# Kernel optimization log

Hardware: AMD Instinct MI355X
Metric: run time of the kernel (lower is better)

The kernel has to match this reference:

```python
import jax, jax.numpy as jnp
import numpy as np

B = 8
H_IN, W_IN = 448, 448
STRIDE = 32
NUM_CLASSES = 20
CONF_THRESH = 0.01
NMS_THRESH = 0.5
HS, WS = H_IN // STRIDE, W_IN // STRIDE  # 14, 14
N_CELLS = HS * WS  # 196
CHANNELS = [3, 64, 128, 256, 512, 512]
HEAD_OUT = 1 + NUM_CLASSES + 4  # 25


def _conv(x, w, stride):
    return jax.lax.conv_general_dilated(
        x, w, (stride, stride), 'SAME',
        dimension_numbers=('NCHW', 'OIHW', 'NCHW'))


def _create_grid():
    gy, gx = jnp.meshgrid(jnp.arange(HS), jnp.arange(WS), indexing='ij')
    return jnp.stack([gx, gy], -1).reshape(1, N_CELLS, 2).astype(jnp.float32)


def _iou_matrix(boxes):
    # boxes: [N,4] xyxy -> [N,N] pairwise IoU
    x1, y1, x2, y2 = boxes[:, 0], boxes[:, 1], boxes[:, 2], boxes[:, 3]
    area = jnp.maximum(x2 - x1, 0.0) * jnp.maximum(y2 - y1, 0.0)
    ix1 = jnp.maximum(x1[:, None], x1[None, :])
    iy1 = jnp.maximum(y1[:, None], y1[None, :])
    ix2 = jnp.minimum(x2[:, None], x2[None, :])
    iy2 = jnp.minimum(y2[:, None], y2[None, :])
    inter = jnp.maximum(ix2 - ix1, 0.0) * jnp.maximum(iy2 - iy1, 0.0)
    return inter / (area[:, None] + area[None, :] - inter + 1e-14)


def _nms_keep(scores, iou):
    # greedy per-class NMS; scores [N], iou [N,N] -> bool keep mask [N]
    order = jnp.argsort(-scores)
    iou_s = iou[order][:, order]
    idx = jnp.arange(N_CELLS)
    valid = scores[order] > CONF_THRESH

    def body(i, keep):
        sup = (iou_s[i] > NMS_THRESH) & (idx > i) & keep[i]
        return keep & (~sup)

    keep = jax.lax.fori_loop(0, N_CELLS, body, valid)
    return jnp.zeros(N_CELLS, bool).at[order].set(keep)


def setup_inputs() -> dict:
    key = jax.random.key(0)
    ks = jax.random.split(key, 8)
    x = jax.random.normal(ks[0], (B, 3, H_IN, W_IN), dtype=jnp.float32)
    params = {}
    for i in range(5):
        cin, cout = CHANNELS[i], CHANNELS[i + 1]
        std = np.sqrt(2.0 / (cin * 9))
        params[f'w{i+1}'] = jax.random.normal(ks[i + 1], (cout, cin, 3, 3), dtype=jnp.float32) * std
    std = np.sqrt(2.0 / CHANNELS[-1])
    params['w_head'] = jax.random.normal(ks[6], (HEAD_OUT, CHANNELS[-1], 1, 1), dtype=jnp.float32) * std
    return {'x': x, **params}


def reference(x, w1, w2, w3, w4, w5, w_head):
    # backbone: 5 stride-2 conv+relu stages -> stride 32
    h = x
    for w in (w1, w2, w3, w4, w5):
        h = jax.nn.relu(_conv(h, w, 2))
    pred = _conv(h, w_head, 1)                      # [B, 25, 14, 14]
    pred = pred.reshape(B, HEAD_OUT, N_CELLS).transpose(0, 2, 1)  # [B, N, 25]

    conf = jax.nn.sigmoid(pred[..., 0:1])                              # [B,N,1]
    cls_scores = jax.nn.softmax(pred[..., 1:1 + NUM_CLASSES], -1) * conf  # [B,N,C]
    txtytwth = pred[..., 1 + NUM_CLASSES:]                             # [B,N,4]

    grid = _create_grid()                                              # [1,N,2]
    xy = (jax.nn.sigmoid(txtytwth[..., :2]) + grid) * STRIDE
    wh = jnp.exp(txtytwth[..., 2:]) * STRIDE
    scale = jnp.array([W_IN, H_IN, W_IN, H_IN], dtype=jnp.float32)
    boxes = jnp.concatenate([xy - wh * 0.5, xy + wh * 0.5], -1) / scale
    boxes = jnp.clip(boxes, 0.0, 1.0)                                  # [B,N,4]

    iou = jax.vmap(_iou_matrix)(boxes)                                 # [B,N,N]
    # per-class NMS, vmapped over classes then batch
    nms_c = jax.vmap(_nms_keep, in_axes=(-1, None), out_axes=-1)       # [N,C]
    keep = jax.vmap(nms_c, in_axes=(0, 0))(cls_scores, iou)            # [B,N,C]
    final_scores = cls_scores * keep
    return jnp.concatenate([boxes, final_scores], -1)                  # [B,N,4+C]
```

## Files before the change

### kernel.cpp

```cpp
#include <hip/hip_runtime.h>
#include <math.h>

#define BATCH 8
#define NCELLS 196
#define NCLS 20
#define HEADC 25

typedef __attribute__((ext_vector_type(8))) short short8;
typedef __attribute__((ext_vector_type(4))) float f32x4;
#define MFMA16(a,b,c) __builtin_amdgcn_mfma_f32_16x16x32_bf16(a,b,c,0,0,0)

__device__ __forceinline__ unsigned short f2bf(float x) {
    union { float f; unsigned u; } a; a.f = x;
    unsigned r = a.u + 0x7FFFu + ((a.u >> 16) & 1u);
    return (unsigned short)(r >> 16);
}
__device__ __forceinline__ float bf2f(unsigned short h) {
    union { unsigned u; float f; } a; a.u = ((unsigned)h) << 16;
    return a.f;
}
__device__ __forceinline__ void split_bf(float x, unsigned short& h, unsigned short& l) {
    h = f2bf(x);
    l = f2bf(x - bf2f(h));
}

template<int CIN, int COUT>
__global__ void prep_w(const float* __restrict__ w, unsigned short* __restrict__ whi,
                       unsigned short* __restrict__ wlo) {
    constexpr int G = COUT / 16, CH = CIN / 32;
    int idx = blockIdx.x * 256 + threadIdx.x;
    if (idx >= 9 * CIN * COUT) return;
    int j    = idx & 7;
    int lane = (idx >> 3) & 63;
    int fg   = idx >> 9;
    int g    = fg % G;
    int fc   = fg / G;
    int chunk = fc % CH;
    int plane = fc / CH;
    int m = lane & 15, quad = lane >> 4;
    int co = g * 16 + m;
    int ci = chunk * 32 + quad * 8 + j;
    int ky = plane / 3, kx = plane % 3;
    float v = w[((co * CIN + ci) * 3 + ky) * 3 + kx];
    unsigned short h, l; split_bf(v, h, l);
    whi[idx] = h; wlo[idx] = l;
}

__global__ void conv1_kernel(const float* __restrict__ x, const float* __restrict__ w1,
                             unsigned short* __restrict__ ohi, unsigned short* __restrict__ olo) {
    __shared__ float sW[27][64];
    __shared__ float sX[3][3][66];
    int bid = blockIdx.x;
    int xseg = bid % 7;  bid /= 7;
    int oy   = bid % 224;
    int b    = bid / 224;
    int ox0  = xseg * 32;

    for (int e = threadIdx.x; e < 1728; e += 256) {
        int k = e >> 6, co = e & 63;
        sW[k][co] = w1[co * 27 + k];
    }
    for (int e = threadIdx.x; e < 594; e += 256) {
        int ci = e / 198;
        int r  = e - ci * 198;
        int ky = r / 66;
        int lx = r - ky * 66;
        int iy = 2 * oy + ky;
        int ix = 2 * ox0 + lx;
        float v = 0.f;
        if (lx < 65 && iy < 448 && ix < 448)
            v = x[(((size_t)b * 3 + ci) * 448 + iy) * 448 + ix];
        sX[ci][ky][lx] = v;
    }
    __syncthreads();

    int pxl = threadIdx.x >> 3;
    int cog = threadIdx.x & 7;
    float acc[8] = {0.f,0.f,0.f,0.f,0.f,0.f,0.f,0.f};
    #pragma unroll
    for (int ci = 0; ci < 3; ci++) {
        #pragma unroll
        for (int ky = 0; ky < 3; ky++) {
            const float* row = sX[ci][ky];
            #pragma unroll
            for (int kx = 0; kx < 3; kx++) {
                float iv = row[2 * pxl + kx];
                int k = (ci * 3 + ky) * 3 + kx;
                float4 wa = *(const float4*)&sW[k][cog * 8];
                float4 wb = *(const float4*)&sW[k][cog * 8 + 4];
                acc[0] += wa.x * iv; acc[1] += wa.y * iv; acc[2] += wa.z * iv; acc[3] += wa.w * iv;
                acc[4] += wb.x * iv; acc[5] += wb.y * iv; acc[6] += wb.z * iv; acc[7] += wb.w * iv;
            }
        }
    }
    union { unsigned short u[8]; uint4 v; } ph, pl;
    #pragma unroll
    for (int u = 0; u < 8; u++) {
        float v = fmaxf(acc[u], 0.f);
        split_bf(v, ph.u[u], pl.u[u]);
    }
    size_t base = ((size_t)(b * 224 + oy) * 224 + ox0 + pxl) * 64 + cog * 8;
    *(uint4*)&ohi[base] = ph.v;
    *(uint4*)&olo[base] = pl.v;
}

template<int CIN, int COUT, int HIN, int WIN, int KSPLIT, bool PARTIAL>
__launch_bounds__(256, 4)
__global__ void conv_mfma(const unsigned short* __restrict__ ahi, const unsigned short* __restrict__ alo,
                          const unsigned short* __restrict__ whi, const unsigned short* __restrict__ wlo,
                          unsigned short* __restrict__ ohi, unsigned short* __restrict__ olo,
                          float* __restrict__ part) {
    constexpr int HOUT = HIN / 2, WOUT = WIN / 2;
    constexpr int TX = (WOUT + 7) / 8, TY = (HOUT + 7) / 8;
    constexpr int COG = COUT / 128;
    constexpr int CH_TOT = CIN / 32;
    constexpr int CH = CH_TOT / KSPLIT;
    constexpr int G = COUT / 16;
    constexpr int PLANE_E = 17 * 17 * 32;
    constexpr size_t PSZ = (size_t)BATCH * HOUT * WOUT * COUT;

    __shared__ __align__(16) unsigned short sA[2 * PLANE_E];

    int bid = blockIdx.x;
    int ks  = bid % KSPLIT; bid /= KSPLIT;
    int txi = bid % TX;     bid /= TX;
    int tyi = bid % TY;     bid /= TY;
    int cg  = bid % COG;
    int b   = bid / COG;
    int oy0 = tyi * 8, ox0 = txi * 8;
    int iy0 = oy0 * 2, ix0 = ox0 * 2;

    int tid = threadIdx.x;
    int w   = tid >> 6;
    int lane = tid & 63;
    int n = lane & 15, quad = lane >> 4;

    int oyl[4], oxl[4], pbase[4];
    #pragma unroll
    for (int nt = 0; nt < 4; nt++) {
        int oyq = nt >> 1, oxq = nt & 1;
        int oy_off = oyq * 4 + (n >> 2);
        int ox_off = oxq * 4 + (n & 3);
        oyl[nt] = oy0 + oy_off;
        oxl[nt] = ox0 + ox_off;
        pbase[nt] = 2 * oy_off * 17 + 2 * ox_off;
    }

    f32x4 zero = {0.f, 0.f, 0.f, 0.f};
    f32x4 acc[2][4];
    #pragma unroll
    for (int ct = 0; ct < 2; ct++)
        #pragma unroll
        for (int nt = 0; nt < 4; nt++) acc[ct][nt] = zero;

    int g0 = cg * 8 + w * 2;

    for (int ch = 0; ch < CH; ch++) {
        int chunk = ks * CH + ch;
        int ci0 = chunk * 32;
        __syncthreads();
        for (int e = tid; e < 17 * 17 * 8; e += 256) {
            int pxi = e >> 3, grp = e & 7;
            int liy = pxi / 17, lix = pxi - liy * 17;
            int iy = iy0 + liy, ix = ix0 + lix;
            uint4 v = make_uint4(0u, 0u, 0u, 0u);
            if (iy < HIN && ix < WIN) {
                const unsigned short* src = ((grp & 4) ? alo : ahi)
                    + ((size_t)(b * HIN + iy) * WIN + ix) * CIN + ci0 + (grp & 3) * 8;
                v = *(const uint4*)src;
            }
            int u = pxi * 4 + ((grp & 3) ^ ((pxi >> 1) & 3));
            *(uint4*)&sA[((grp >> 2) ? PLANE_E : 0) + u * 8] = v;
        }
        __syncthreads();
        #pragma unroll
        for (int pl = 0; pl < 9; pl++) {
            int ky = pl / 3, kx = pl % 3;
            size_t fbase = ((size_t)(pl * CH_TOT + chunk) * G + g0) * 512 + lane * 8;
            short8 Ah0 = *(const short8*)(whi + fbase);
            short8 Ah1 = *(const short8*)(whi + fbase + 512);
            short8 Al0 = *(const short8*)(wlo + fbase);
            short8 Al1 = *(const short8*)(wlo + fbase + 512);
            int dp = ky * 17 + kx;
            #pragma unroll
            for (int nt = 0; nt < 4; nt++) {
                int p = pbase[nt] + dp;
                int u = p * 4 + (quad ^ ((p >> 1) & 3));
                short8 Bh = *(const short8*)&sA[u * 8];
                short8 Bl = *(const short8*)&sA[PLANE_E + u * 8];
                acc[0][nt] = MFMA16(Ah0, Bh, acc[0][nt]);
                acc[0][nt] = MFMA16(Ah0, Bl, acc[0][nt]);
                acc[0][nt] = MFMA16(Al0, Bh, acc[0][nt]);
                acc[1][nt] = MFMA16(Ah1, Bh, acc[1][nt]);
                acc[1][nt] = MFMA16(Ah1, Bl, acc[1][nt]);
                acc[1][nt] = MFMA16(Al1, Bh, acc[1][nt]);
            }
        }
    }
    int cob = cg * 128 + w * 32;
    #pragma unroll
    for (int ct = 0; ct < 2; ct++) {
        #pragma unroll
        for (int nt = 0; nt < 4; nt++) {
            if (oyl[nt] >= HOUT || oxl[nt] >= WOUT) continue;
            size_t base = ((size_t)(b * HOUT + oyl[nt]) * WOUT + oxl[nt]) * COUT
                          + cob + ct * 16 + quad * 4;
            if (PARTIAL) {
                *(f32x4*)&part[(size_t)ks * PSZ + base] = acc[ct][nt];
            } else {
                unsigned long long h64 = 0ull, l64 = 0ull;
                #pragma unroll
                for (int r = 0; r < 4; r++) {
                    float v = fmaxf(acc[ct][nt][r], 0.f);
                    unsigned short hh, ll; split_bf(v, hh, ll);
                    h64 |= ((unsigned long long)hh) << (16 * r);
                    l64 |= ((unsigned long long)ll) << (16 * r);
                }
                *(unsigned long long*)&ohi[base] = h64;
                *(unsigned long long*)&olo[base] = l64;
            }
        }
    }
}

template<int KS>
__global__ void reduceN_split(const float* __restrict__ p, unsigned short* __restrict__ oh,
                              unsigned short* __restrict__ ol, int n) {
    int n4 = n >> 2;
    int i = blockIdx.x * 256 + threadIdx.x;
    if (i >= n4) return;
    const float4* p4 = (const float4*)p;
    float4 s = p4[i];
    #pragma unroll
    for (int k = 1; k < KS; k++) {
        float4 t = p4[i + (size_t)k * n4];
        s.x += t.x; s.y += t.y; s.z += t.z; s.w += t.w;
    }
    float v[4] = { fmaxf(s.x,0.f), fmaxf(s.y,0.f), fmaxf(s.z,0.f), fmaxf(s.w,0.f) };
    unsigned long long h64 = 0ull, l64 = 0ull;
    #pragma unroll
    for (int r = 0; r < 4; r++) {
        unsigned short hh, ll; split_bf(v[r], hh, ll);
        h64 |= ((unsigned long long)hh) << (16 * r);
        l64 |= ((unsigned long long)ll) << (16 * r);
    }
    *(unsigned long long*)&oh[i * 4] = h64;
    *(unsigned long long*)&ol[i * 4] = l64;
}

__global__ void head_kernel(const unsigned short* __restrict__ ah, const unsigned short* __restrict__ al,
                            const float* __restrict__ wh, float* __restrict__ pred) {
    int wave = threadIdx.x >> 6;
    int lane = threadIdx.x & 63;
    int cellid = blockIdx.x * 4 + wave;
    float acc[HEADC];
    #pragma unroll
    for (int c = 0; c < HEADC; c++) acc[c] = 0.f;
    for (int it = 0; it < 8; it++) {
        int ci = it * 64 + lane;
        size_t idx = (size_t)cellid * 512 + ci;
        float a = bf2f(ah[idx]) + bf2f(al[idx]);
        #pragma unroll
        for (int c = 0; c < HEADC; c++) acc[c] += a * wh[c * 512 + ci];
    }
    #pragma unroll
    for (int c = 0; c < HEADC; c++) {
        float v = acc[c];
        v += __shfl_down(v, 32); v += __shfl_down(v, 16); v += __shfl_down(v, 8);
        v += __shfl_down(v, 4);  v += __shfl_down(v, 2);  v += __shfl_down(v, 1);
        if (lane == 0) pred[(size_t)cellid * HEADC + c] = v;
    }
}

__global__ void decode_kernel(const float* __restrict__ pred, float* __restrict__ out,
                              float* __restrict__ cls) {
    int i = blockIdx.x * 256 + threadIdx.x;
    if (i >= BATCH * NCELLS) return;
    const float* p = pred + (size_t)i * HEADC;
    int cell = i % NCELLS;
    int gx = cell % 14, gy = cell / 14;
    float conf = 1.f / (1.f + expf(-p[0]));
    float m = p[1];
    #pragma unroll
    for (int c = 1; c < NCLS; c++) m = fmaxf(m, p[1 + c]);
    float e[NCLS], s = 0.f;
    #pragma unroll
    for (int c = 0; c < NCLS; c++) { e[c] = expf(p[1 + c] - m); s += e[c]; }
    float inv = conf / s;
    #pragma unroll
    for (int c = 0; c < NCLS; c++) cls[(size_t)i * NCLS + c] = e[c] * inv;
    float cx = (1.f / (1.f + expf(-p[21])) + gx) * 32.f;
    float cy = (1.f / (1.f + expf(-p[22])) + gy) * 32.f;
    float w  = expf(p[23]) * 32.f;
    float h  = expf(p[24]) * 32.f;
    float x1 = (cx - 0.5f * w) / 448.f, y1 = (cy - 0.5f * h) / 448.f;
    float x2 = (cx + 0.5f * w) / 448.f, y2 = (cy + 0.5f * h) / 448.f;
    x1 = fminf(fmaxf(x1, 0.f), 1.f); y1 = fminf(fmaxf(y1, 0.f), 1.f);
    x2 = fminf(fmaxf(x2, 0.f), 1.f); y2 = fminf(fmaxf(y2, 0.f), 1.f);
    float* o = out + (size_t)i * 24;
    o[0] = x1; o[1] = y1; o[2] = x2; o[3] = y2;
}

__global__ void iou_kernel(const float* __restrict__ out, float* __restrict__ iou) {
    int idx = blockIdx.x * 256 + threadIdx.x;
    if (idx >= BATCH * NCELLS * NCELLS) return;
    int j = idx % NCELLS;
    int i = (idx / NCELLS) % NCELLS;
    int b = idx / (NCELLS * NCELLS);
    const float* bi = out + (((size_t)b * NCELLS) + i) * 24;
    const float* bj = out + (((size_t)b * NCELLS) + j) * 24;
    float ai = fmaxf(bi[2] - bi[0], 0.f) * fmaxf(bi[3] - bi[1], 0.f);
    float aj = fmaxf(bj[2] - bj[0], 0.f) * fmaxf(bj[3] - bj[1], 0.f);
    float ix1 = fmaxf(bi[0], bj[0]), iy1 = fmaxf(bi[1], bj[1]);
    float ix2 = fminf(bi[2], bj[2]), iy2 = fminf(bi[3], bj[3]);
    float inter = fmaxf(ix2 - ix1, 0.f) * fmaxf(iy2 - iy1, 0.f);
    iou[idx] = inter / (ai + aj - inter + 1e-14f);
}

__global__ void nms_kernel(const float* __restrict__ cls, const float* __restrict__ iou,
                           float* __restrict__ out) {
    int b = blockIdx.x / NCLS;
    int c = blockIdx.x % NCLS;
    __shared__ float sc[NCELLS];
    __shared__ float ssort[NCELLS];
    __shared__ int   ord[NCELLS];
    __shared__ int   kp[NCELLS];
    int j = threadIdx.x;
    float sj = 0.f;
    if (j < NCELLS) {
        sj = cls[(((size_t)b * NCELLS) + j) * NCLS + c];
        sc[j] = sj;
    }
    __syncthreads();
    if (j < NCELLS) {
        int r = 0;
        for (int k = 0; k < NCELLS; k++) {
            float sk = sc[k];
            r += (sk > sj) || (sk == sj && k < j);
        }
        ord[r] = j; ssort[r] = sj; kp[r] = (sj > 0.01f) ? 1 : 0;
    }
    __syncthreads();
    int myo = (j < NCELLS) ? ord[j] : 0;
    const float* iob = iou + (size_t)b * NCELLS * NCELLS;
    for (int i = 0; i < NCELLS; i++) {
        __syncthreads();
        if (!kp[i]) continue;
        if (j > i && j < NCELLS && kp[j]) {
            if (iob[ord[i] * NCELLS + myo] > 0.5f) kp[j] = 0;
        }
    }
    __syncthreads();
    if (j < NCELLS)
        out[(((size_t)b * NCELLS) + ord[j]) * 24 + 4 + c] = kp[j] ? ssort[j] : 0.f;
}

extern "C" void kernel_launch(void* const* d_in, const int* in_sizes, int n_in,
                              void* d_out, int out_size, void* d_ws, size_t ws_size,
                              hipStream_t stream) {
    const float* x  = (const float*)d_in[0];
    const float* w1 = (const float*)d_in[1];
    const float* w2 = (const float*)d_in[2];
    const float* w3 = (const float*)d_in[3];
    const float* w4 = (const float*)d_in[4];
    const float* w5 = (const float*)d_in[5];
    const float* wh = (const float*)d_in[6];
    float* out = (float*)d_out;
    char* base = (char*)d_ws;

    unsigned short* a1h = (unsigned short*)(base);
    unsigned short* a1l = a1h + 25690112;
    unsigned short* a3h = (unsigned short*)(base);
    unsigned short* a3l = a3h + 6422528;
    float* part4 = (float*)(base + 25690112);
    float* part5 = (float*)(base);
    unsigned short* a5h = (unsigned short*)(base + 51380224);
    unsigned short* a5l = a5h + 802816;
    float* pred = (float*)(base + 54589440);
    float* clsb = (float*)(base + 54746240);
    float* ioub = (float*)(base + 54871680);
    unsigned short* a2h = (unsigned short*)(base + 102760448);
    unsigned short* a2l = a2h + 12845056;
    unsigned short* a4h = (unsigned short*)(base + 102760448);
    unsigned short* a4l = a4h + 3211264;
    unsigned short* w2h = (unsigned short*)(base + 154140672);
    unsigned short* w3h = w2h + 73728;
    unsigned short* w4h = w3h + 294912;
    unsigned short* w5h = w4h + 1179648;
    unsigned short* w2l = (unsigned short*)(base + 161955840);
    unsigned short* w3l = w2l + 73728;
    unsigned short* w4l = w3l + 294912;
    unsigned short* w5l = w4l + 1179648;

    prep_w<64, 128> <<<288,  256, 0, stream>>>(w2, w2h, w2l);
    prep_w<128, 256><<<1152, 256, 0, stream>>>(w3, w3h, w3l);
    prep_w<256, 512><<<4608, 256, 0, stream>>>(w4, w4h, w4l);
    prep_w<512, 512><<<9216, 256, 0, stream>>>(w5, w5h, w5l);

    conv1_kernel<<<12544, 256, 0, stream>>>(x, w1, a1h, a1l);

    conv_mfma<64, 128, 224, 224, 1, false><<<1568, 256, 0, stream>>>(
        a1h, a1l, w2h, w2l, a2h, a2l, nullptr);
    conv_mfma<128, 256, 112, 112, 1, false><<<784, 256, 0, stream>>>(
        a2h, a2l, w3h, w3l, a3h, a3l, nullptr);
    conv_mfma<256, 512, 56, 56, 2, true><<<1024, 256, 0, stream>>>(
        a3h, a3l, w4h, w4l, nullptr, nullptr, part4);
    reduceN_split<2><<<3136, 256, 0, stream>>>(part4, a4h, a4l, 3211264);
    conv_mfma<512, 512, 28, 28, 8, true><<<1024, 256, 0, stream>>>(
        a4h, a4l, w5h, w5l, nullptr, nullptr, part5);
    reduceN_split<8><<<784, 256, 0, stream>>>(part5, a5h, a5l, 802816);

    head_kernel<<<392, 256, 0, stream>>>(a5h, a5l, wh, pred);
    decode_kernel<<<7, 256, 0, stream>>>(pred, out, clsb);
    iou_kernel<<<1201, 256, 0, stream>>>(out, ioub);
    nms_kernel<<<160, 256, 0, stream>>>(clsb, ioub, out);
}
```

Measured before the change: 468.7 us.

## Replace serialized NMS loop with parallel suppression bitmasks and register scan

The per-class NMS kernel previously ran 196 serial iterations, each with a block-wide barrier and a dependent global IoU load. It now builds a 196x256-bit suppression mask in shared memory, with each wave computing rows in parallel via ballot. Each wave then runs the greedy keep scan redundantly on 64-bit register masks, with no barriers. This trades the serial sync chain for extra IoU reads of masked-out rows and a per-wave sequential bit scan.

Result: faster. 445.6 us (-4.9%).

```diff
diff --git a/kernel.cpp b/kernel.cpp
--- a/kernel.cpp
+++ b/kernel.cpp
@@ -324,8 +324,10 @@
     __shared__ float sc[NCELLS];
     __shared__ float ssort[NCELLS];
     __shared__ int   ord[NCELLS];
-    __shared__ int   kp[NCELLS];
+    __shared__ __align__(16) unsigned long long smask[NCELLS][4];
     int j = threadIdx.x;
+    int lane = j & 63;
+    int w = j >> 6;
     float sj = 0.f;
     if (j < NCELLS) {
         sj = cls[(((size_t)b * NCELLS) + j) * NCLS + c];
@@ -338,21 +340,54 @@
             float sk = sc[k];
             r += (sk > sj) || (sk == sj && k < j);
         }
-        ord[r] = j; ssort[r] = sj; kp[r] = (sj > 0.01f) ? 1 : 0;
+        ord[r] = j; ssort[r] = sj;
     }
     __syncthreads();
-    int myo = (j < NCELLS) ? ord[j] : 0;
     const float* iob = iou + (size_t)b * NCELLS * NCELLS;
-    for (int i = 0; i < NCELLS; i++) {
-        __syncthreads();
-        if (!kp[i]) continue;
-        if (j > i && j < NCELLS && kp[j]) {
-            if (iob[ord[i] * NCELLS + myo] > 0.5f) kp[j] = 0;
+    int oc[4];
+    #pragma unroll
+    for (int k = 0; k < 4; k++) {
+        int cidx = k * 64 + lane;
+        oc[k] = (cidx < NCELLS) ? ord[cidx] : 0;
+    }
+    for (int i = w; i < NCELLS; i += 4) {
+        const float* rowp = iob + ord[i] * NCELLS;
+        #pragma unroll
+        for (int k = 0; k < 4; k++) {
+            int cidx = k * 64 + lane;
+            bool sup = false;
+            if (cidx < NCELLS && cidx > i)
+                sup = rowp[oc[k]] > 0.5f;
+            unsigned long long m = __ballot(sup);
+            if (lane == 0) smask[i][k] = m;
         }
     }
     __syncthreads();
-    if (j < NCELLS)
-        out[(((size_t)b * NCELLS) + ord[j]) * 24 + 4 + c] = kp[j] ? ssort[j] : 0.f;
+    unsigned long long keep[4];
+    #pragma unroll
+    for (int k = 0; k < 4; k++) {
+        int cidx = k * 64 + lane;
+        bool valid = (cidx < NCELLS) && (ssort[cidx] > 0.01f);
+        keep[k] = __ballot(valid);
+    }
+    #pragma unroll
+    for (int wi = 0; wi < 4; wi++) {
+        int base = wi * 64;
+        int lim = (NCELLS - base < 64) ? (NCELLS - base) : 64;
+        for (int t = 0; t < lim; t++) {
+            if ((keep[wi] >> t) & 1ull) {
+                int i = base + t;
+                keep[0] &= ~smask[i][0];
+                keep[1] &= ~smask[i][1];
+                keep[2] &= ~smask[i][2];
+                keep[3] &= ~smask[i][3];
+            }
+        }
+    }
+    if (j < NCELLS) {
+        bool kept = (keep[w] >> lane) & 1ull;
+        out[(((size_t)b * NCELLS) + ord[j]) * 24 + 4 + c] = kept ? ssort[j] : 0.f;
+    }
 }
 
 extern "C" void kernel_launch(void* const* d_in, const int* in_sizes, int n_in,
```
